# Kernel tuning notes

Measured on AMD Instinct MI355X. Metric: run time of the kernel, lower is better.

The kernel has to match this reference:

```python
import jax, jax.numpy as jnp
import numpy as np

B, S, D = 2, 2048, 1024
H = 16
HD = D // H
RANK = 8
ALPHA = 8.0
NEG = -1e9


def setup_inputs() -> dict:
    key = jax.random.key(0)
    ks = jax.random.split(key, 7)
    inv = 1.0 / np.sqrt(D)
    return {
        "x": jax.random.normal(ks[0], (B, S, D), dtype=jnp.float32),
        "W_qkv": jax.random.normal(ks[1], (D, 3 * D), dtype=jnp.float32) * inv,
        "b_qkv": jax.random.normal(ks[2], (3 * D,), dtype=jnp.float32) * 0.02,
        # LoRA: A ~ N(0, 1/rank) per torch init; B is zeros at init but given
        # small values here so the LoRA path is exercised numerically.
        "A_lora": jax.random.normal(ks[3], (D, RANK), dtype=jnp.float32) / np.sqrt(RANK),
        "B_lora": jax.random.normal(ks[4], (RANK, 3 * D), dtype=jnp.float32) * 0.02,
        "W_proj": jax.random.normal(ks[5], (D, D), dtype=jnp.float32) * inv,
        "b_proj": jax.random.normal(ks[6], (D,), dtype=jnp.float32) * 0.02,
    }


def _split_heads(t):
    # [B, S, D] -> [B, H, S, HD]
    return t.reshape(B, S, H, HD).transpose(0, 2, 1, 3)


def reference(x, W_qkv, b_qkv, A_lora, B_lora, W_proj, b_proj):
    # c_attn: LoRALayer -> base linear + alpha * (x @ A @ B)
    qkv = x @ W_qkv + b_qkv + (x @ A_lora @ B_lora) * ALPHA  # [B, S, 3D]
    q, k, v = jnp.split(qkv, 3, axis=-1)
    q, k, v = _split_heads(q), _split_heads(k), _split_heads(v)

    # SelfAttentionFunction: QK^T, add mask, THEN divide by sqrt(head_dim)
    causal = jnp.tril(jnp.ones((S, S), dtype=bool))
    mask = jnp.where(causal, 0.0, NEG).astype(x.dtype)  # [S, S] additive
    scores = (jnp.einsum("bhqd,bhkd->bhqk", q, k) + mask) / jnp.sqrt(
        jnp.asarray(HD, dtype=x.dtype)
    )
    attn = jax.nn.softmax(scores, axis=-1)  # [B, H, S, S]
    ctx = jnp.einsum("bhqk,bhkd->bhqd", attn, v)  # [B, H, S, HD]

    # merge heads -> c_proj (plain LoRaLinear: x @ W + b)
    ctx = ctx.transpose(0, 2, 1, 3).reshape(B, S, D)
    out = ctx @ W_proj + b_proj
    return out
```

## Files before the change

kernel.cpp:

```cpp
#include <hip/hip_runtime.h>
#include <hip/hip_bf16.h>


#define BB    2
#define SS    2048
#define DD    1024
#define HH    16
#define HDIM  64
#define N3    3072
#define MR    4096

typedef short short8 __attribute__((ext_vector_type(8)));
typedef short s16x4 __attribute__((ext_vector_type(4)));
typedef float f32x4 __attribute__((ext_vector_type(4)));

#define MFMA16(a, b, c) __builtin_amdgcn_mfma_f32_16x16x32_bf16((a), (b), (c), 0, 0, 0)

__device__ __forceinline__ float b2f(short s) {
    union { unsigned int u; float f; } c;
    c.u = ((unsigned int)(unsigned short)s) << 16;
    return c.f;
}
__device__ __forceinline__ short f2b(float f) {
    union { __hip_bfloat16 h; short s; } c;
    c.h = __float2bfloat16(f);
    return c.s;
}
struct HiLo { short hi, lo; };
__device__ __forceinline__ HiLo split2(float v) {
    HiLo r;
    r.hi = f2b(v);
    r.lo = f2b(v - b2f(r.hi));
    return r;
}

__device__ __forceinline__ void gl_lds16(const void* g, void* l) {
    __builtin_amdgcn_global_load_lds(
        (const __attribute__((address_space(1))) void*)g,
        (__attribute__((address_space(3))) void*)l, 16, 0, 0);
}


__global__ __launch_bounds__(256) void prep_all(
    const float* __restrict__ X, short* __restrict__ Xhi, short* __restrict__ Xlo,
    const float* __restrict__ Wq, const float* __restrict__ Al,
    const float* __restrict__ Bl, short* __restrict__ Wqhi, short* __restrict__ Wqlo,
    const float* __restrict__ Wp, short* __restrict__ Wphi, short* __restrict__ Wplo)
{
    __shared__ float sw[64][68];
    __shared__ float sa[64][8];
    __shared__ float sb[8][64];
    int bid = blockIdx.x;
    int tid = threadIdx.x;

    if (bid >= 1024) {
        int id = bid - 1024;
        int kc = id & 31, p = id >> 5;
        int row = tid >> 1, half = tid & 1;
        const float* src = &X[((size_t)p * 128 + row) * 1024 + kc * 32 + half * 16];
        f32x4 v[4];
#pragma unroll
        for (int u = 0; u < 4; u++) v[u] = *(const f32x4*)(src + u * 4);
        size_t base = ((size_t)p * 32 + kc) * 4096 + (size_t)(half * 2) * 1024 + row * 8;
#pragma unroll
        for (int u = 0; u < 2; u++) {
            short8 h8, l8;
#pragma unroll
            for (int j = 0; j < 8; j++) {
                HiLo hl = split2(v[u * 2 + (j >> 2)][j & 3]);
                h8[j] = hl.hi; l8[j] = hl.lo;
            }
            *(short8*)&Xhi[base + u * 1024] = h8;
            *(short8*)&Xlo[base + u * 1024] = l8;
        }
        return;
    }

    const float* W; short *Whi, *Wlo;
    int N, lora, bx, by;
    if (bid < 768) {
        W = Wq; Whi = Wqhi; Wlo = Wqlo; N = N3; lora = 1;
        bx = bid % 48; by = bid / 48;
    } else {
        int id = bid - 768;
        W = Wp; Whi = Wphi; Wlo = Wplo; N = DD; lora = 0;
        bx = id & 15; by = id >> 4;
    }
    int n0 = bx * 64, k0 = by * 64;
#pragma unroll
    for (int p = 0; p < 4; p++) {
        int idx = p * 256 + tid;
        int kr = idx >> 4, ch = idx & 15;
        *(f32x4*)&sw[kr][ch * 4] = *(const f32x4*)&W[(size_t)(k0 + kr) * N + n0 + ch * 4];
    }
    if (lora) {
        if (tid < 64) {
#pragma unroll
            for (int r = 0; r < 8; r++) sa[tid][r] = Al[(k0 + tid) * 8 + r];
        } else if (tid < 128) {
            int c = tid - 64;
#pragma unroll
            for (int r = 0; r < 8; r++) sb[r][c] = Bl[(size_t)r * N + n0 + c];
        }
    }
    __syncthreads();
#pragma unroll
    for (int p = 0; p < 2; p++) {
        int idx = p * 256 + tid;
        int nr = idx >> 3, ch = idx & 7;
        short8 h8, l8;
#pragma unroll
        for (int j = 0; j < 8; j++) {
            int k = ch * 8 + j;
            float v = sw[k][nr];
            if (lora) {
                float a2 = 0.f;
#pragma unroll
                for (int r = 0; r < 8; r++) a2 += sa[k][r] * sb[r][nr];
                v += 8.0f * a2;
            }
            HiLo hl = split2(v);
            h8[j] = hl.hi;
            l8[j] = hl.lo;
        }
        int n = n0 + nr;
        int kchunk = (k0 >> 5) + (ch >> 2);
        size_t off = ((size_t)(n >> 7) * 32 + kchunk) * 4096 +
                     (size_t)(ch & 3) * 1024 + (n & 127) * 8;
        *(short8*)&Whi[off] = h8;
        *(short8*)&Wlo[off] = l8;
    }
}

__global__ __launch_bounds__(256) void gemm3(
    const short* __restrict__ Ahi, const short* __restrict__ Alo,
    const short* __restrict__ Bhi, const short* __restrict__ Blo,
    const float* __restrict__ bias,
    float* __restrict__ qf, short* __restrict__ khi, short* __restrict__ klo,
    short* __restrict__ vt, float* __restrict__ outf32, int N, int mode)
{
    __shared__ short lds[2][4][4][128][8];
    int tid = threadIdx.x;
    int wav = tid >> 6, lane = tid & 63;
    int l15 = lane & 15, q4 = lane >> 4;
    int wm = wav & 1, wn = wav >> 1;
    int n0 = blockIdx.x * 128, m0 = blockIdx.y * 128;

    const short* ga_h = Ahi + ((size_t)blockIdx.y * 32) * 4096 + tid * 8;
    const short* ga_l = Alo + ((size_t)blockIdx.y * 32) * 4096 + tid * 8;
    const short* gb_h = Bhi + ((size_t)blockIdx.x * 32) * 4096 + tid * 8;
    const short* gb_l = Blo + ((size_t)blockIdx.x * 32) * 4096 + tid * 8;
    short* l0 = &lds[0][0][0][0][0] + tid * 8;

    f32x4 acc[4][4] = {};

#define STAGE(kc_, buf_)                                         \
    {                                                            \
        int koff_ = (kc_) * 4096;                                \
        short* lb_ = l0 + (buf_) * 16384;                        \
        gl_lds16(ga_h + koff_,        lb_);                      \
        gl_lds16(ga_h + koff_ + 2048, lb_ + 2048);               \
        gl_lds16(ga_l + koff_,        lb_ + 4096);               \
        gl_lds16(ga_l + koff_ + 2048, lb_ + 6144);               \
        gl_lds16(gb_h + koff_,        lb_ + 8192);               \
        gl_lds16(gb_h + koff_ + 2048, lb_ + 10240);              \
        gl_lds16(gb_l + koff_,        lb_ + 12288);              \
        gl_lds16(gb_l + koff_ + 2048, lb_ + 14336);              \
    }

    STAGE(0, 0);
    __syncthreads();

    for (int kc = 0; kc < 32; ++kc) {
        int cur = kc & 1;
        if (kc + 1 < 32) STAGE(kc + 1, cur ^ 1);
        short8 ah[4], al_[4], bh[4], bl[4];
#pragma unroll
        for (int i = 0; i < 4; i++) {
            ah[i]  = *(short8*)&lds[cur][0][q4][wm * 64 + i * 16 + l15][0];
            al_[i] = *(short8*)&lds[cur][1][q4][wm * 64 + i * 16 + l15][0];
            bh[i]  = *(short8*)&lds[cur][2][q4][wn * 64 + i * 16 + l15][0];
            bl[i]  = *(short8*)&lds[cur][3][q4][wn * 64 + i * 16 + l15][0];
        }
#pragma unroll
        for (int mi = 0; mi < 4; mi++)
#pragma unroll
            for (int ni = 0; ni < 4; ni++) {
                acc[mi][ni] = MFMA16(ah[mi], bh[ni], acc[mi][ni]);
                acc[mi][ni] = MFMA16(ah[mi], bl[ni], acc[mi][ni]);
                acc[mi][ni] = MFMA16(al_[mi], bh[ni], acc[mi][ni]);
            }
        __syncthreads();
    }
#undef STAGE
#pragma unroll
    for (int ni = 0; ni < 4; ni++) {
        int n = n0 + wn * 64 + ni * 16 + l15;
        float bv = bias[n];
#pragma unroll
        for (int mi = 0; mi < 4; mi++) {
            int mbase = m0 + wm * 64 + mi * 16 + q4 * 4;
#pragma unroll
            for (int r = 0; r < 4; r++) {
                int m = mbase + r;
                float v = acc[mi][ni][r] + bv;
                if (mode != 0) {
                    outf32[(size_t)m * 1024 + n] = v;
                } else if (n0 < 1024) {
                    qf[(size_t)m * 1024 + n] = v * 0.125f;
                } else if (n0 < 2048) {
                    int kk = n - 1024, hh = kk >> 6, hd = kk & 63;
                    int bb_ = m >> 11, s = m & 2047;
                    int oct = hd >> 3;
                    size_t base = ((size_t)((bb_ << 4) + hh) * 32 + (s >> 6)) * 4096
                                  + (size_t)oct * 512 + ((s & 63) ^ oct) * 8 + (hd & 7);
                    HiLo hl = split2(v);
                    khi[base] = hl.hi;
                    klo[base] = hl.lo;
                } else {
                    int kk = n - 2048, hh = kk >> 6, hd = kk & 63;
                    int bb_ = m >> 11, s = m & 2047;
                    int oct = (s >> 3) & 7;
                    size_t base = ((size_t)((bb_ << 4) + hh) * 32 + (s >> 6)) * 4096
                                  + (size_t)oct * 512 + (hd ^ oct) * 8 + (s & 7);
                    vt[base] = f2b(v);
                }
            }
        }
    }
}

__global__ __launch_bounds__(256) void attn_mfma(const float* __restrict__ qf,
                                                 const short* __restrict__ khi,
                                                 const short* __restrict__ klo,
                                                 const short* __restrict__ vtg,
                                                 short* __restrict__ ctxhi,
                                                 short* __restrict__ ctxlo) {
    __shared__ short KhL[2][4096];
    __shared__ short KlL[2][4096];
    __shared__ short VtL[2][4096];
    __shared__ short Pt[4][8][17][8];

    int h = blockIdx.y, b = blockIdx.z;
    int tid = threadIdx.x, wav = tid >> 6, lane = tid & 63;
    int l15 = lane & 15, q4 = lane >> 4;
    const float* bq = qf + (size_t)b * SS * 1024;
    size_t hb = (size_t)((b * 16 + h) * 32) * 4096;
    const short* gkh = khi + hb;
    const short* gkl = klo + hb;
    const short* gvt = vtg + hb;
    int t8 = tid * 8;

#define ISSUE(c, buf)                                                   \
    {                                                                   \
        size_t co_ = (size_t)(c) * 4096 + t8;                           \
        gl_lds16(gkh + co_,        &KhL[buf][t8]);                      \
        gl_lds16(gkh + co_ + 2048, &KhL[buf][t8 + 2048]);               \
        gl_lds16(gkl + co_,        &KlL[buf][t8]);                      \
        gl_lds16(gkl + co_ + 2048, &KlL[buf][t8 + 2048]);               \
        gl_lds16(gvt + co_,        &VtL[buf][t8]);                      \
        gl_lds16(gvt + co_ + 2048, &VtL[buf][t8 + 2048]);               \
    }

    for (int t = 0; t < 2; ++t) {
        int qt = t ? (int)blockIdx.x : 31 - (int)blockIdx.x;
        int qb = qt * 64;

        size_t qoff = (size_t)(qb + wav * 16 + l15) * 1024 + h * 64;
        short8 q0h, q0l, q1h, q1l;
        {
            f32x4 a0 = *(const f32x4*)&bq[qoff + q4 * 8];
            f32x4 a1 = *(const f32x4*)&bq[qoff + q4 * 8 + 4];
            f32x4 c0 = *(const f32x4*)&bq[qoff + 32 + q4 * 8];
            f32x4 c1 = *(const f32x4*)&bq[qoff + 32 + q4 * 8 + 4];
#pragma unroll
            for (int j = 0; j < 4; j++) {
                HiLo u = split2(a0[j]); q0h[j] = u.hi; q0l[j] = u.lo;
                HiLo v = split2(a1[j]); q0h[4 + j] = v.hi; q0l[4 + j] = v.lo;
                HiLo w = split2(c0[j]); q1h[j] = w.hi; q1l[j] = w.lo;
                HiLo z = split2(c1[j]); q1h[4 + j] = z.hi; q1l[4 + j] = z.lo;
            }
        }

        f32x4 o[4] = {};
        float msc = -1e30f;
        float lsc = 0.f;
        int nch = qt + 1;

        ISSUE(0, 0);
        __syncthreads();

        for (int c = 0; c < nch; ++c) {
            int cur = c & 1;
            int k0 = c * 64;

            if (c + 1 < nch) ISSUE(c + 1, cur ^ 1);

            f32x4 s[4];
            __builtin_amdgcn_s_setprio(1);
#pragma unroll
            for (int g = 0; g < 4; g++) {
                int ko  = q4 * 512 + ((g * 16 + l15) ^ q4) * 8;
                int ko2 = (4 + q4) * 512 + ((g * 16 + l15) ^ (4 + q4)) * 8;
                short8 k0h_ = *(short8*)&KhL[cur][ko];
                short8 k0l_ = *(short8*)&KlL[cur][ko];
                short8 k1h_ = *(short8*)&KhL[cur][ko2];
                short8 k1l_ = *(short8*)&KlL[cur][ko2];
                f32x4 acc = {};
                acc = MFMA16(k0h_, q0h, acc);
                acc = MFMA16(k0l_, q0h, acc);
                acc = MFMA16(k0h_, q0l, acc);
                acc = MFMA16(k1h_, q1h, acc);
                acc = MFMA16(k1l_, q1h, acc);
                acc = MFMA16(k1h_, q1l, acc);
                s[g] = acc;
            }
            __builtin_amdgcn_s_setprio(0);

            if (c == qt) {
                int q = qb + wav * 16 + l15;
#pragma unroll
                for (int g = 0; g < 4; g++)
#pragma unroll
                    for (int r = 0; r < 4; r++)
                        if (k0 + g * 16 + q4 * 4 + r > q) s[g][r] = -1e30f;
            }
            f32x4 mx4 = s[0];
#pragma unroll
            for (int g = 1; g < 4; g++) {
                mx4[0] = fmaxf(mx4[0], s[g][0]); mx4[1] = fmaxf(mx4[1], s[g][1]);
                mx4[2] = fmaxf(mx4[2], s[g][2]); mx4[3] = fmaxf(mx4[3], s[g][3]);
            }
            float mx = fmaxf(fmaxf(mx4[0], mx4[1]), fmaxf(mx4[2], mx4[3]));
            mx = fmaxf(mx, __shfl_xor(mx, 16, 64));
            mx = fmaxf(mx, __shfl_xor(mx, 32, 64));
            float mn = fmaxf(msc, mx);
            f32x4 ps = {};
#pragma unroll
            for (int g = 0; g < 4; g++) {
                s16x4 pb;
#pragma unroll
                for (int r = 0; r < 4; r++) {
                    float p = __expf(s[g][r] - mn);
                    ps[r] += p;
                    pb[r] = f2b(p);
                }
                *(s16x4*)&Pt[wav][g * 2 + (q4 >> 1)][l15][(q4 & 1) * 4] = pb;
            }
            float sm = (ps[0] + ps[1]) + (ps[2] + ps[3]);
            sm += __shfl_xor(sm, 16, 64);
            sm += __shfl_xor(sm, 32, 64);
            float alpha_s = __expf(msc - mn);
            msc = mn;
            lsc = lsc * alpha_s + sm;
            float al0 = __shfl(alpha_s, q4 * 4 + 0, 64);
            float al1 = __shfl(alpha_s, q4 * 4 + 1, 64);
            float al2 = __shfl(alpha_s, q4 * 4 + 2, 64);
            float al3 = __shfl(alpha_s, q4 * 4 + 3, 64);

            short8 pf0 = *(short8*)&Pt[wav][q4][l15][0];
            short8 pf1 = *(short8*)&Pt[wav][4 + q4][l15][0];
            __builtin_amdgcn_s_setprio(1);
#pragma unroll
            for (int gg = 0; gg < 4; gg++) {
                int vo  = q4 * 512 + ((gg * 16 + l15) ^ q4) * 8;
                int vo2 = (4 + q4) * 512 + ((gg * 16 + l15) ^ (4 + q4)) * 8;
                short8 vf0 = *(short8*)&VtL[cur][vo];
                short8 vf1 = *(short8*)&VtL[cur][vo2];
                f32x4 tt = o[gg];
                tt[0] *= al0; tt[1] *= al1; tt[2] *= al2; tt[3] *= al3;
                tt = MFMA16(pf0, vf0, tt);
                tt = MFMA16(pf1, vf1, tt);
                o[gg] = tt;
            }
            __builtin_amdgcn_s_setprio(0);

            __syncthreads();
        }

        float ls0 = __shfl(lsc, q4 * 4 + 0, 64);
        float ls1 = __shfl(lsc, q4 * 4 + 1, 64);
        float ls2 = __shfl(lsc, q4 * 4 + 2, 64);
        float ls3 = __shfl(lsc, q4 * 4 + 3, 64);
        float lsr[4] = {ls0, ls1, ls2, ls3};
#pragma unroll
        for (int gg = 0; gg < 4; gg++)
#pragma unroll
            for (int r = 0; r < 4; r++) {
                int q = qb + wav * 16 + q4 * 4 + r;
                int mrow = b * SS + q;
                int k = h * 64 + gg * 16 + l15;
                HiLo hl = split2(o[gg][r] / lsr[r]);
                size_t off = ((size_t)(mrow >> 7) * 32 + (k >> 5)) * 4096 +
                             (size_t)((k >> 3) & 3) * 1024 + (mrow & 127) * 8 + (k & 7);
                ctxhi[off] = hl.hi;
                ctxlo[off] = hl.lo;
            }
    }
#undef ISSUE
}

extern "C" void kernel_launch(void* const* d_in, const int* in_sizes, int n_in,
                              void* d_out, int out_size, void* d_ws, size_t ws_size,
                              hipStream_t stream) {
    const float* x  = (const float*)d_in[0];
    const float* Wq = (const float*)d_in[1];
    const float* bq = (const float*)d_in[2];
    const float* Al = (const float*)d_in[3];
    const float* Bl = (const float*)d_in[4];
    const float* Wp = (const float*)d_in[5];
    const float* bp = (const float*)d_in[6];

    char* ws = (char*)d_ws;
    float* qf     = (float*)(ws);
    short* khi    = (short*)(ws + (size_t)16 * 1024 * 1024);
    short* klo    = (short*)(ws + (size_t)24 * 1024 * 1024);
    short* vt     = (short*)(ws + (size_t)32 * 1024 * 1024);
    short* wpt_hi = (short*)(ws + (size_t)40 * 1024 * 1024);
    short* wpt_lo = (short*)(ws + (size_t)42 * 1024 * 1024);
    short* wqt_hi = (short*)(ws + (size_t)44 * 1024 * 1024);
    short* wqt_lo = (short*)(ws + (size_t)50 * 1024 * 1024);
    short* xhi    = (short*)(ws + (size_t)56 * 1024 * 1024);
    short* xlo    = (short*)(ws + (size_t)64 * 1024 * 1024);
    short* ctxhi  = (short*)(ws + (size_t)44 * 1024 * 1024);
    short* ctxlo  = (short*)(ws + (size_t)52 * 1024 * 1024);

    hipLaunchKernelGGL(prep_all, dim3(2048), dim3(256), 0, stream,
                       x, xhi, xlo, Wq, Al, Bl, wqt_hi, wqt_lo,
                       Wp, wpt_hi, wpt_lo);
    hipLaunchKernelGGL(gemm3, dim3(N3 / 128, MR / 128), dim3(256), 0, stream,
                       xhi, xlo, wqt_hi, wqt_lo, bq,
                       qf, khi, klo, vt, (float*)nullptr, N3, 0);
    hipLaunchKernelGGL(attn_mfma, dim3(SS / 128, HH, BB), dim3(256), 0, stream,
                       qf, khi, klo, vt, ctxhi, ctxlo);
    hipLaunchKernelGGL(gemm3, dim3(DD / 128, MR / 128), dim3(256), 0, stream,
                       ctxhi, ctxlo, wpt_hi, wpt_lo, bp,
                       (float*)nullptr, (short*)nullptr, (short*)nullptr,
                       (short*)nullptr, (float*)d_out, DD, 1);
}
```

Baseline: 286.0 us.

## Process paired query tiles in one K/V sweep to share loaded chunks

Instead of two sequential passes over K/V for the paired query tiles (31-x and x), the block now loads each K/V chunk once and runs the tile step for both query tiles. This cuts global-to-LDS traffic and barriers for the shorter tile. The P staging buffer is also halved by writing and consuming P in two halves. In exchange, register pressure rises because two sets of Q fragments and accumulators stay live, which could hurt occupancy or cause spills.

```diff
diff --git a/kernel.cpp b/kernel.cpp
--- a/kernel.cpp
+++ b/kernel.cpp
@@ -239,7 +239,7 @@
     __shared__ short KhL[2][4096];
     __shared__ short KlL[2][4096];
     __shared__ short VtL[2][4096];
-    __shared__ short Pt[4][8][17][8];
+    __shared__ short Pt[4][4][17][8];
 
     int h = blockIdx.y, b = blockIdx.z;
     int tid = threadIdx.x, wav = tid >> 6, lane = tid & 63;
@@ -262,142 +262,156 @@
         gl_lds16(gvt + co_ + 2048, &VtL[buf][t8 + 2048]);               \
     }
 
-    for (int t = 0; t < 2; ++t) {
-        int qt = t ? (int)blockIdx.x : 31 - (int)blockIdx.x;
-        int qb = qt * 64;
-
-        size_t qoff = (size_t)(qb + wav * 16 + l15) * 1024 + h * 64;
-        short8 q0h, q0l, q1h, q1l;
-        {
-            f32x4 a0 = *(const f32x4*)&bq[qoff + q4 * 8];
-            f32x4 a1 = *(const f32x4*)&bq[qoff + q4 * 8 + 4];
-            f32x4 c0 = *(const f32x4*)&bq[qoff + 32 + q4 * 8];
-            f32x4 c1 = *(const f32x4*)&bq[qoff + 32 + q4 * 8 + 4];
-#pragma unroll
-            for (int j = 0; j < 4; j++) {
-                HiLo u = split2(a0[j]); q0h[j] = u.hi; q0l[j] = u.lo;
-                HiLo v = split2(a1[j]); q0h[4 + j] = v.hi; q0l[4 + j] = v.lo;
-                HiLo w = split2(c0[j]); q1h[j] = w.hi; q1l[j] = w.lo;
-                HiLo z = split2(c1[j]); q1h[4 + j] = z.hi; q1l[4 + j] = z.lo;
-            }
-        }
-
-        f32x4 o[4] = {};
-        float msc = -1e30f;
-        float lsc = 0.f;
-        int nch = qt + 1;
-
-        ISSUE(0, 0);
+#define LOADQ(qb_, q0h_, q0l_, q1h_, q1l_)                                   \
+    {                                                                        \
+        size_t qoff_ = (size_t)((qb_) + wav * 16 + l15) * 1024 + h * 64;     \
+        f32x4 a0_ = *(const f32x4*)&bq[qoff_ + q4 * 8];                      \
+        f32x4 a1_ = *(const f32x4*)&bq[qoff_ + q4 * 8 + 4];                  \
+        f32x4 c0_ = *(const f32x4*)&bq[qoff_ + 32 + q4 * 8];                 \
+        f32x4 c1_ = *(const f32x4*)&bq[qoff_ + 32 + q4 * 8 + 4];             \
+        _Pragma("unroll") for (int j_ = 0; j_ < 4; j_++) {                   \
+            HiLo u_ = split2(a0_[j_]); q0h_[j_] = u_.hi; q0l_[j_] = u_.lo;   \
+            HiLo v_ = split2(a1_[j_]); q0h_[4 + j_] = v_.hi; q0l_[4 + j_] = v_.lo; \
+            HiLo w_ = split2(c0_[j_]); q1h_[j_] = w_.hi; q1l_[j_] = w_.lo;   \
+            HiLo z_ = split2(c1_[j_]); q1h_[4 + j_] = z_.hi; q1l_[4 + j_] = z_.lo; \
+        }                                                                    \
+    }
+
+#define TILE_STEP(qt_, qb_, q0h_, q0l_, q1h_, q1l_, o_, msc_, lsc_)          \
+    {                                                                        \
+        f32x4 s_[4];                                                         \
+        __builtin_amdgcn_s_setprio(1);                                       \
+        _Pragma("unroll") for (int g_ = 0; g_ < 4; g_++) {                   \
+            int ko_  = q4 * 512 + ((g_ * 16 + l15) ^ q4) * 8;                \
+            int ko2_ = (4 + q4) * 512 + ((g_ * 16 + l15) ^ (4 + q4)) * 8;    \
+            short8 k0h_ = *(short8*)&KhL[cur][ko_];                          \
+            short8 k0l_ = *(short8*)&KlL[cur][ko_];                          \
+            short8 k1h_ = *(short8*)&KhL[cur][ko2_];                         \
+            short8 k1l_ = *(short8*)&KlL[cur][ko2_];                         \
+            f32x4 acc_ = {};                                                 \
+            acc_ = MFMA16(k0h_, q0h_, acc_);                                 \
+            acc_ = MFMA16(k0l_, q0h_, acc_);                                 \
+            acc_ = MFMA16(k0h_, q0l_, acc_);                                 \
+            acc_ = MFMA16(k1h_, q1h_, acc_);                                 \
+            acc_ = MFMA16(k1l_, q1h_, acc_);                                 \
+            acc_ = MFMA16(k1h_, q1l_, acc_);                                 \
+            s_[g_] = acc_;                                                   \
+        }                                                                    \
+        __builtin_amdgcn_s_setprio(0);                                       \
+        if (c == (qt_)) {                                                    \
+            int q_ = (qb_) + wav * 16 + l15;                                 \
+            _Pragma("unroll") for (int g_ = 0; g_ < 4; g_++)                 \
+                _Pragma("unroll") for (int r_ = 0; r_ < 4; r_++)             \
+                    if (k0 + g_ * 16 + q4 * 4 + r_ > q_) s_[g_][r_] = -1e30f;\
+        }                                                                    \
+        f32x4 mx4_ = s_[0];                                                  \
+        _Pragma("unroll") for (int g_ = 1; g_ < 4; g_++) {                   \
+            mx4_[0] = fmaxf(mx4_[0], s_[g_][0]);                             \
+            mx4_[1] = fmaxf(mx4_[1], s_[g_][1]);                             \
+            mx4_[2] = fmaxf(mx4_[2], s_[g_][2]);                             \
+            mx4_[3] = fmaxf(mx4_[3], s_[g_][3]);                             \
+        }                                                                    \
+        float mx_ = fmaxf(fmaxf(mx4_[0], mx4_[1]), fmaxf(mx4_[2], mx4_[3]));\
+        mx_ = fmaxf(mx_, __shfl_xor(mx_, 16, 64));                           \
+        mx_ = fmaxf(mx_, __shfl_xor(mx_, 32, 64));                           \
+        float mn_ = fmaxf(msc_, mx_);                                        \
+        f32x4 ps_ = {};                                                      \
+        s16x4 pb_[4];                                                        \
+        _Pragma("unroll") for (int g_ = 0; g_ < 4; g_++) {                   \
+            _Pragma("unroll") for (int r_ = 0; r_ < 4; r_++) {               \
+                float p_ = __expf(s_[g_][r_] - mn_);                         \
+                ps_[r_] += p_;                                               \
+                pb_[g_][r_] = f2b(p_);                                       \
+            }                                                                \
+        }                                                                    \
+        float sm_ = (ps_[0] + ps_[1]) + (ps_[2] + ps_[3]);                   \
+        sm_ += __shfl_xor(sm_, 16, 64);                                      \
+        sm_ += __shfl_xor(sm_, 32, 64);                                      \
+        float alpha_ = __expf(msc_ - mn_);                                   \
+        msc_ = mn_;                                                          \
+        lsc_ = lsc_ * alpha_ + sm_;                                          \
+        float al0_ = __shfl(alpha_, q4 * 4 + 0, 64);                         \
+        float al1_ = __shfl(alpha_, q4 * 4 + 1, 64);                         \
+        float al2_ = __shfl(alpha_, q4 * 4 + 2, 64);                         \
+        float al3_ = __shfl(alpha_, q4 * 4 + 3, 64);                         \
+        *(s16x4*)&Pt[wav][0 + (q4 >> 1)][l15][(q4 & 1) * 4] = pb_[0];        \
+        *(s16x4*)&Pt[wav][2 + (q4 >> 1)][l15][(q4 & 1) * 4] = pb_[1];        \
+        short8 pf0_ = *(short8*)&Pt[wav][q4][l15][0];                        \
+        __builtin_amdgcn_s_setprio(1);                                       \
+        _Pragma("unroll") for (int gg_ = 0; gg_ < 4; gg_++) {                \
+            int vo_ = q4 * 512 + ((gg_ * 16 + l15) ^ q4) * 8;                \
+            short8 vf0_ = *(short8*)&VtL[cur][vo_];                          \
+            f32x4 tt_ = o_[gg_];                                             \
+            tt_[0] *= al0_; tt_[1] *= al1_; tt_[2] *= al2_; tt_[3] *= al3_;  \
+            o_[gg_] = MFMA16(pf0_, vf0_, tt_);                               \
+        }                                                                    \
+        __builtin_amdgcn_s_setprio(0);                                       \
+        *(s16x4*)&Pt[wav][0 + (q4 >> 1)][l15][(q4 & 1) * 4] = pb_[2];        \
+        *(s16x4*)&Pt[wav][2 + (q4 >> 1)][l15][(q4 & 1) * 4] = pb_[3];        \
+        short8 pf1_ = *(short8*)&Pt[wav][q4][l15][0];                        \
+        __builtin_amdgcn_s_setprio(1);                                       \
+        _Pragma("unroll") for (int gg_ = 0; gg_ < 4; gg_++) {                \
+            int vo2_ = (4 + q4) * 512 + ((gg_ * 16 + l15) ^ (4 + q4)) * 8;   \
+            short8 vf1_ = *(short8*)&VtL[cur][vo2_];                         \
+            o_[gg_] = MFMA16(pf1_, vf1_, o_[gg_]);                           \
+        }                                                                    \
+        __builtin_amdgcn_s_setprio(0);                                       \
+    }
+
+#define WRITE_CTX(qb_, o_, lsc_)                                             \
+    {                                                                        \
+        float ls0_ = __shfl(lsc_, q4 * 4 + 0, 64);                           \
+        float ls1_ = __shfl(lsc_, q4 * 4 + 1, 64);                           \
+        float ls2_ = __shfl(lsc_, q4 * 4 + 2, 64);                           \
+        float ls3_ = __shfl(lsc_, q4 * 4 + 3, 64);                           \
+        float lsr_[4] = {ls0_, ls1_, ls2_, ls3_};                            \
+        _Pragma("unroll") for (int gg_ = 0; gg_ < 4; gg_++)                  \
+            _Pragma("unroll") for (int r_ = 0; r_ < 4; r_++) {               \
+                int q_ = (qb_) + wav * 16 + q4 * 4 + r_;                     \
+                int mrow_ = b * SS + q_;                                     \
+                int k_ = h * 64 + gg_ * 16 + l15;                            \
+                HiLo hl_ = split2(o_[gg_][r_] / lsr_[r_]);                   \
+                size_t off_ = ((size_t)(mrow_ >> 7) * 32 + (k_ >> 5)) * 4096 \
+                    + (size_t)((k_ >> 3) & 3) * 1024 + (mrow_ & 127) * 8 + (k_ & 7); \
+                ctxhi[off_] = hl_.hi;                                        \
+                ctxlo[off_] = hl_.lo;                                        \
+            }                                                                \
+    }
+
+    int x = blockIdx.x;
+    int qtA = 31 - x, qtB = x;
+    int qbA = qtA * 64, qbB = qtB * 64;
+
+    short8 qA0h, qA0l, qA1h, qA1l, qB0h, qB0l, qB1h, qB1l;
+    LOADQ(qbA, qA0h, qA0l, qA1h, qA1l);
+    LOADQ(qbB, qB0h, qB0l, qB1h, qB1l);
+
+    f32x4 oA[4] = {}, oB[4] = {};
+    float mscA = -1e30f, lscA = 0.f, mscB = -1e30f, lscB = 0.f;
+    int nch = qtA + 1;
+
+    ISSUE(0, 0);
+    __syncthreads();
+
+    for (int c = 0; c < nch; ++c) {
+        int cur = c & 1;
+        int k0 = c * 64;
+
+        if (c + 1 < nch) ISSUE(c + 1, cur ^ 1);
+
+        TILE_STEP(qtA, qbA, qA0h, qA0l, qA1h, qA1l, oA, mscA, lscA);
+        if (c <= qtB)
+            TILE_STEP(qtB, qbB, qB0h, qB0l, qB1h, qB1l, oB, mscB, lscB);
+
         __syncthreads();
-
-        for (int c = 0; c < nch; ++c) {
-            int cur = c & 1;
-            int k0 = c * 64;
-
-            if (c + 1 < nch) ISSUE(c + 1, cur ^ 1);
-
-            f32x4 s[4];
-            __builtin_amdgcn_s_setprio(1);
-#pragma unroll
-            for (int g = 0; g < 4; g++) {
-                int ko  = q4 * 512 + ((g * 16 + l15) ^ q4) * 8;
-                int ko2 = (4 + q4) * 512 + ((g * 16 + l15) ^ (4 + q4)) * 8;
-                short8 k0h_ = *(short8*)&KhL[cur][ko];
-                short8 k0l_ = *(short8*)&KlL[cur][ko];
-                short8 k1h_ = *(short8*)&KhL[cur][ko2];
-                short8 k1l_ = *(short8*)&KlL[cur][ko2];
-                f32x4 acc = {};
-                acc = MFMA16(k0h_, q0h, acc);
-                acc = MFMA16(k0l_, q0h, acc);
-                acc = MFMA16(k0h_, q0l, acc);
-                acc = MFMA16(k1h_, q1h, acc);
-                acc = MFMA16(k1l_, q1h, acc);
-                acc = MFMA16(k1h_, q1l, acc);
-                s[g] = acc;
-            }
-            __builtin_amdgcn_s_setprio(0);
-
-            if (c == qt) {
-                int q = qb + wav * 16 + l15;
-#pragma unroll
-                for (int g = 0; g < 4; g++)
-#pragma unroll
-                    for (int r = 0; r < 4; r++)
-                        if (k0 + g * 16 + q4 * 4 + r > q) s[g][r] = -1e30f;
-            }
-            f32x4 mx4 = s[0];
-#pragma unroll
-            for (int g = 1; g < 4; g++) {
-                mx4[0] = fmaxf(mx4[0], s[g][0]); mx4[1] = fmaxf(mx4[1], s[g][1]);
-                mx4[2] = fmaxf(mx4[2], s[g][2]); mx4[3] = fmaxf(mx4[3], s[g][3]);
-            }
-            float mx = fmaxf(fmaxf(mx4[0], mx4[1]), fmaxf(mx4[2], mx4[3]));
-            mx = fmaxf(mx, __shfl_xor(mx, 16, 64));
-            mx = fmaxf(mx, __shfl_xor(mx, 32, 64));
-            float mn = fmaxf(msc, mx);
-            f32x4 ps = {};
-#pragma unroll
-            for (int g = 0; g < 4; g++) {
-                s16x4 pb;
-#pragma unroll
-                for (int r = 0; r < 4; r++) {
-                    float p = __expf(s[g][r] - mn);
-                    ps[r] += p;
-                    pb[r] = f2b(p);
-                }
-                *(s16x4*)&Pt[wav][g * 2 + (q4 >> 1)][l15][(q4 & 1) * 4] = pb;
-            }
-            float sm = (ps[0] + ps[1]) + (ps[2] + ps[3]);
-            sm += __shfl_xor(sm, 16, 64);
-            sm += __shfl_xor(sm, 32, 64);
-            float alpha_s = __expf(msc - mn);
-            msc = mn;
-            lsc = lsc * alpha_s + sm;
-            float al0 = __shfl(alpha_s, q4 * 4 + 0, 64);
-            float al1 = __shfl(alpha_s, q4 * 4 + 1, 64);
-            float al2 = __shfl(alpha_s, q4 * 4 + 2, 64);
-            float al3 = __shfl(alpha_s, q4 * 4 + 3, 64);
-
-            short8 pf0 = *(short8*)&Pt[wav][q4][l15][0];
-            short8 pf1 = *(short8*)&Pt[wav][4 + q4][l15][0];
-            __builtin_amdgcn_s_setprio(1);
-#pragma unroll
-            for (int gg = 0; gg < 4; gg++) {
-                int vo  = q4 * 512 + ((gg * 16 + l15) ^ q4) * 8;
-                int vo2 = (4 + q4) * 512 + ((gg * 16 + l15) ^ (4 + q4)) * 8;
-                short8 vf0 = *(short8*)&VtL[cur][vo];
-                short8 vf1 = *(short8*)&VtL[cur][vo2];
-                f32x4 tt = o[gg];
-                tt[0] *= al0; tt[1] *= al1; tt[2] *= al2; tt[3] *= al3;
-                tt = MFMA16(pf0, vf0, tt);
-                tt = MFMA16(pf1, vf1, tt);
-                o[gg] = tt;
-            }
-            __builtin_amdgcn_s_setprio(0);
-
-            __syncthreads();
-        }
-
-        float ls0 = __shfl(lsc, q4 * 4 + 0, 64);
-        float ls1 = __shfl(lsc, q4 * 4 + 1, 64);
-        float ls2 = __shfl(lsc, q4 * 4 + 2, 64);
-        float ls3 = __shfl(lsc, q4 * 4 + 3, 64);
-        float lsr[4] = {ls0, ls1, ls2, ls3};
-#pragma unroll
-        for (int gg = 0; gg < 4; gg++)
-#pragma unroll
-            for (int r = 0; r < 4; r++) {
-                int q = qb + wav * 16 + q4 * 4 + r;
-                int mrow = b * SS + q;
-                int k = h * 64 + gg * 16 + l15;
-                HiLo hl = split2(o[gg][r] / lsr[r]);
-                size_t off = ((size_t)(mrow >> 7) * 32 + (k >> 5)) * 4096 +
-                             (size_t)((k >> 3) & 3) * 1024 + (mrow & 127) * 8 + (k & 7);
-                ctxhi[off] = hl.hi;
-                ctxlo[off] = hl.lo;
-            }
-    }
+    }
+
+    WRITE_CTX(qbA, oA, lscA);
+    WRITE_CTX(qbB, oB, lscB);
 #undef ISSUE
+#undef LOADQ
+#undef TILE_STEP
+#undef WRITE_CTX
 }
 
 extern "C" void kernel_launch(void* const* d_in, const int* in_sizes, int n_in,
```

Measured after the change: 271.6 us. -5.0%, faster.
